# Kernel optimization log

Hardware: AMD Instinct MI355X
Metric: run time of the kernel (lower is better)

## Reference

```python
import jax, jax.numpy as jnp
import numpy as np

WINDOW = 16  # signature_window_size
D = 6        # input_path_dim


def _mlp(x, Ws, bs, final_act):
    for W, b in zip(Ws[:-1], bs[:-1]):
        x = jax.nn.softplus(W @ x + b)
    return final_act(Ws[-1] @ x + bs[-1])


def _windowed_logsig(xs):
    """Depth-2 log-signature of each window of the (piecewise-linear) path.
    Returns level-1 increments [n, D] and Levy areas [n, D, D] (antisymmetric)."""
    dx = xs[1:] - xs[:-1]                              # [T-1, D]
    n = dx.shape[0] // WINDOW
    dxw = dx[: n * WINDOW].reshape(n, WINDOW, D)
    lvl1 = dxw.sum(axis=1)                             # [n, D]
    cum = jnp.cumsum(dxw, axis=1) - dxw                # exclusive prefix sums
    cross = jnp.einsum('nwi,nwj->nij', cum, dxw)
    area = 0.5 * (cross - jnp.swapaxes(cross, 1, 2))   # [n, D, D]
    return lvl1, area


def setup_inputs() -> dict:
    key = jax.random.key(0)
    ks = jax.random.split(key, 9)
    S, H, OUT = 128, 128, 10
    B, T = 8, 513

    def lin(k, o, i):
        return jax.random.normal(k, (o, i), jnp.float32) / np.sqrt(i)

    return {
        'x': jax.random.normal(ks[0], (B, T, D), jnp.float32),
        'W_i0': lin(ks[1], H, D), 'b_i0': jnp.zeros((H,), jnp.float32),
        'W_i1': lin(ks[2], H, H), 'b_i1': jnp.zeros((H,), jnp.float32),
        'W_i2': lin(ks[3], S, H), 'b_i2': jnp.zeros((S,), jnp.float32),
        'W_v0': lin(ks[4], H, S), 'b_v0': jnp.zeros((H,), jnp.float32),
        'W_v1': lin(ks[5], H, H), 'b_v1': jnp.zeros((H,), jnp.float32),
        'W_v2': lin(ks[6], D * S, H), 'b_v2': jnp.zeros((D * S,), jnp.float32),
        'W_r': lin(ks[7], OUT, S), 'b_r': jnp.zeros((OUT,), jnp.float32),
    }


def reference(x, W_i0, b_i0, W_i1, b_i1, W_i2, b_i2,
              W_v0, b_v0, W_v1, b_v1, W_v2, b_v2, W_r, b_r):
    S = W_i2.shape[0]
    init_mlp = lambda z: _mlp(z, (W_i0, W_i1, W_i2), (b_i0, b_i1, b_i2), lambda u: u)
    # Vector fields V_i: R^S -> R^S, one per input channel (split_multi_vector_field)
    vf = lambda h: _mlp(h, (W_v0, W_v1, W_v2), (b_v0, b_v1, b_v2), jnp.tanh).reshape(D, S)
    mask = jnp.triu(jnp.ones((D, D), x.dtype), 1)  # Lyndon words i<j at depth 2

    def single(xs):  # xs: [T, D]
        lvl1, area = _windowed_logsig(xs)
        h0 = init_mlp(xs[0])

        def step(h, sig):
            l1, a = sig
            V = vf(h)                                  # [D, S]
            J = jax.jacfwd(vf)(h)                      # [D, S, S], J[j,b,a]=dV_j[b]/dh[a]
            M = jnp.einsum('jba,ia->ijb', J, V)        # (DV_j)(h) V_i(h)
            brack = M - jnp.swapaxes(M, 0, 1)          # Lie brackets [V_i, V_j](h)
            h_new = h + jnp.einsum('i,ib->b', l1, V) \
                      + jnp.einsum('ij,ijb->b', a * mask, brack)  # log-ODE step
            return h_new, h_new

        _, hist = jax.lax.scan(step, h0, (lvl1, area))
        hist = jnp.concatenate([h0[None], hist], axis=0)   # [n+1, S]
        return hist @ W_r.T + b_r                          # evolving readout

    return jax.vmap(single)(x)
```

## Files before the change

### kernel.cpp

```cpp
#include <hip/hip_runtime.h>
#include <math.h>

#define D    6
#define S    128
#define H    128
#define WIN  16
#define BB   8
#define TT   513
#define NW   32
#define OUTD 10

__device__ float g_lvl1[BB * NW * D];
__device__ float g_area[BB * NW * D * D];
__device__ float g_h0[BB * S];
__device__ float g_hist[BB * (NW + 1) * S];
__device__ float4 g_W2p[3 * 16 * 512];

__device__ __forceinline__ float sp(float x) {
    return (x > 20.f) ? x : log1pf(expf(x));
}
__device__ __forceinline__ float sigm(float x) {
    return 1.f / (1.f + expf(-x));
}
__device__ __forceinline__ float dot4(float4 a, float4 b, float acc) {
    return fmaf(a.x, b.x, fmaf(a.y, b.y, fmaf(a.z, b.z, fmaf(a.w, b.w, acc))));
}

#define O_W0   0
#define O_W1   16384
#define O_PS   32768
#define O_U    35840
#define O_T    36608
#define O_V    37376
#define O_H    38144
#define O_U1   38400
#define O_U2   38528
#define O_SG1  38656
#define O_SG2  38784
#define O_B0   38912
#define O_B1   39040
#define O_SIG  39168
#define O_B2   39256
#define SMTOT  40024

__global__ __launch_bounds__(512) void k_pack(const float* __restrict__ Wv2) {
    const float4* W24 = (const float4*)Wv2;
    int e = blockIdx.x * 512 + threadIdx.x;
    if (e < 3 * 16 * 512) {
        int ptr = e >> 13;
        int rem = e & 8191;
        int i   = rem >> 9;
        int tid = rem & 511;
        int r0 = tid >> 1, kh = tid & 1;
        int row = r0 + ptr * 256;
        g_W2p[e] = W24[row * 32 + kh * 16 + i];
    }
}

__global__ __launch_bounds__(256) void k_sig(
        const float* __restrict__ x,
        const float* __restrict__ Wi0, const float* __restrict__ bi0,
        const float* __restrict__ Wi1, const float* __restrict__ bi1,
        const float* __restrict__ Wi2, const float* __restrict__ bi2) {
    const int b = blockIdx.x;
    const int tid = threadIdx.x;
    __shared__ float dxs[NW][WIN][D];
    __shared__ float cums[NW][WIN][D];
    __shared__ float ua[H], ub[H];

    const float* xb = x + (size_t)b * TT * D;

    if (tid < NW * D) {
        int w = tid / D, i = tid % D;
        float run = 0.f;
        float prev = xb[(w * WIN) * D + i];
        for (int k = 0; k < WIN; ++k) {
            float cur = xb[(w * WIN + k + 1) * D + i];
            float d = cur - prev; prev = cur;
            dxs[w][k][i] = d;
            cums[w][k][i] = run;
            run += d;
        }
        g_lvl1[(b * NW + w) * D + i] = run;
    }
    __syncthreads();
    for (int e = tid; e < NW * D * D; e += blockDim.x) {
        int w = e / (D * D); int rem = e % (D * D);
        int i = rem / D, j = rem % D;
        float s = 0.f;
        for (int k = 0; k < WIN; ++k)
            s += cums[w][k][i] * dxs[w][k][j] - cums[w][k][j] * dxs[w][k][i];
        g_area[(b * NW + w) * (D * D) + rem] = 0.5f * s;
    }
    if (tid < H) {
        float z = bi0[tid];
        for (int k = 0; k < D; ++k) z += Wi0[tid * D + k] * xb[k];
        ua[tid] = sp(z);
    }
    __syncthreads();
    if (tid < H) {
        float z = bi1[tid];
        for (int k = 0; k < H; ++k) z += Wi1[tid * H + k] * ua[k];
        ub[tid] = sp(z);
    }
    __syncthreads();
    if (tid < H) {
        float z = bi2[tid];
        for (int k = 0; k < H; ++k) z += Wi2[tid * H + k] * ub[k];
        g_h0[b * S + tid] = z;
    }
}

__global__ __launch_bounds__(512, 2) void k_scan(
        const float* __restrict__ bv0, const float* __restrict__ bv1,
        const float* __restrict__ bv2,
        const float* __restrict__ Wv0, const float* __restrict__ Wv1) {
    __shared__ float sm[SMTOT];
    const int tid = threadIdx.x;
    const int b = blockIdx.x;
    const int r   = tid & 127;
    const int c4  = tid >> 7;
    const int key = r & 7;
    const int kh = tid & 1;
    const int r0 = tid >> 1, r1 = r0 + 256, r2 = r0 + 512;
    const int jA = tid >> 8, jB = 2 + jA, jC = 4 + jA;

    {
        float4* d = (float4*)(sm + O_W0);
        const float4* s0 = (const float4*)Wv0;
        const float4* s1 = (const float4*)Wv1;
        for (int i = tid; i < 4096; i += 512) { d[i] = s0[i]; d[4096 + i] = s1[i]; }
        sm[O_B2 + tid] = bv2[tid];
        if (tid < 256) sm[O_B2 + 512 + tid] = bv2[512 + tid];
        if (tid < 128) { sm[O_B0 + tid] = bv0[tid]; sm[O_B1 + tid] = bv1[tid]; }
    }
    const float4* WAp = g_W2p + tid;
    const float4* WBp = g_W2p + 8192 + tid;
    const float4* WCp = g_W2p + 16384 + tid;
    if (tid < 128) {
        float h0v = g_h0[b * 128 + tid];
        sm[O_H + tid] = h0v;
        g_hist[(b * (NW + 1)) * 128 + tid] = h0v;
    }
    if (tid >= 448) {
        int q = tid - 448;
        if (q < 42)
            sm[O_SIG + q] = (q < 6) ? g_lvl1[(b * NW) * 6 + q]
                                    : g_area[(b * NW) * 36 + q - 6];
    }
    __syncthreads();

    const float4* W04 = (const float4*)(sm + O_W0);
    const float4* W14 = (const float4*)(sm + O_W1);

    for (int t = 0; t < NW; ++t) {
        float rsig = 0.f;
        if (tid >= 448) {
            int q = tid - 448;
            if (q < 42 && t + 1 < NW)
                rsig = (q < 6) ? g_lvl1[(b * NW + t + 1) * 6 + q]
                               : g_area[(b * NW + t + 1) * 36 + q - 6];
        }
        const int sb = O_SIG + (t & 1) * 44;

        {
            float a = 0.f;
            const float4* H4 = (const float4*)(sm + O_H);
            #pragma unroll
            for (int q = 0; q < 8; ++q) {
                int qq = c4 * 8 + (q ^ key);
                a = dot4(W04[r * 32 + qq], H4[qq], a);
            }
            sm[O_PS + (c4 * 6) * 128 + r] = a;
        }
        __syncthreads();
        if (tid < 128) {
            float z = sm[O_B0 + tid];
            #pragma unroll
            for (int c = 0; c < 4; ++c) z += sm[O_PS + (c * 6) * 128 + tid];
            sm[O_U1 + tid] = sp(z); sm[O_SG1 + tid] = sigm(z);
        }
        __syncthreads();
        {
            float a = 0.f;
            const float4* U14 = (const float4*)(sm + O_U1);
            #pragma unroll
            for (int q = 0; q < 8; ++q) {
                int qq = c4 * 8 + (q ^ key);
                a = dot4(W14[r * 32 + qq], U14[qq], a);
            }
            sm[O_PS + (c4 * 6) * 128 + r] = a;
        }
        __syncthreads();
        if (tid < 128) {
            float z = sm[O_B1 + tid];
            #pragma unroll
            for (int c = 0; c < 4; ++c) z += sm[O_PS + (c * 6) * 128 + tid];
            sm[O_U2 + tid] = sp(z); sm[O_SG2 + tid] = sigm(z);
        }
        __syncthreads();
        {
            float acc0 = 0.f, acc1 = 0.f, acc2 = 0.f;
            const float4* U24 = (const float4*)(sm + O_U2) + kh * 16;
            #pragma unroll 4
            for (int i = 0; i < 16; ++i) {
                float4 u = U24[i];
                acc0 = dot4(WAp[i * 512], u, acc0);
                acc1 = dot4(WBp[i * 512], u, acc1);
                acc2 = dot4(WCp[i * 512], u, acc2);
            }
            sm[O_PS + kh * 768 + r0] = acc0;
            sm[O_PS + kh * 768 + r1] = acc1;
            sm[O_PS + kh * 768 + r2] = acc2;
        }
        __syncthreads();
        {
            sm[O_V + tid] = tanhf(sm[O_B2 + tid] + sm[O_PS + tid] + sm[O_PS + 768 + tid]);
            if (tid < 256) {
                int e = tid + 512;
                sm[O_V + e] = tanhf(sm[O_B2 + e] + sm[O_PS + e] + sm[O_PS + 768 + e]);
            }
        }
        __syncthreads();
        {
            float a0 = 0.f, a1 = 0.f, a2 = 0.f, a3 = 0.f, a4 = 0.f, a5 = 0.f;
            const float4* V4 = (const float4*)(sm + O_V);
            #pragma unroll
            for (int q = 0; q < 8; ++q) {
                int qq = c4 * 8 + (q ^ key);
                float4 w = W04[r * 32 + qq];
                a0 = dot4(w, V4[qq], a0);
                a1 = dot4(w, V4[32 + qq], a1);
                a2 = dot4(w, V4[64 + qq], a2);
                a3 = dot4(w, V4[96 + qq], a3);
                a4 = dot4(w, V4[128 + qq], a4);
                a5 = dot4(w, V4[160 + qq], a5);
            }
            sm[O_PS + (c4 * 6 + 0) * 128 + r] = a0;
            sm[O_PS + (c4 * 6 + 1) * 128 + r] = a1;
            sm[O_PS + (c4 * 6 + 2) * 128 + r] = a2;
            sm[O_PS + (c4 * 6 + 3) * 128 + r] = a3;
            sm[O_PS + (c4 * 6 + 4) * 128 + r] = a4;
            sm[O_PS + (c4 * 6 + 5) * 128 + r] = a5;
        }
        __syncthreads();
        {
            #pragma unroll
            for (int s = 0; s < 2; ++s) {
                int e = tid + s * 512;
                if (s == 0 || tid < 256) {
                    int jj = e >> 7, rr = e & 127;
                    float y0 = sm[O_PS + 0 * 128 + rr] + sm[O_PS + (6 + 0) * 128 + rr]
                             + sm[O_PS + (12 + 0) * 128 + rr] + sm[O_PS + (18 + 0) * 128 + rr];
                    float y1 = sm[O_PS + 1 * 128 + rr] + sm[O_PS + (6 + 1) * 128 + rr]
                             + sm[O_PS + (12 + 1) * 128 + rr] + sm[O_PS + (18 + 1) * 128 + rr];
                    float y2 = sm[O_PS + 2 * 128 + rr] + sm[O_PS + (6 + 2) * 128 + rr]
                             + sm[O_PS + (12 + 2) * 128 + rr] + sm[O_PS + (18 + 2) * 128 + rr];
                    float y3 = sm[O_PS + 3 * 128 + rr] + sm[O_PS + (6 + 3) * 128 + rr]
                             + sm[O_PS + (12 + 3) * 128 + rr] + sm[O_PS + (18 + 3) * 128 + rr];
                    float y4 = sm[O_PS + 4 * 128 + rr] + sm[O_PS + (6 + 4) * 128 + rr]
                             + sm[O_PS + (12 + 4) * 128 + rr] + sm[O_PS + (18 + 4) * 128 + rr];
                    float y5 = sm[O_PS + 5 * 128 + rr] + sm[O_PS + (6 + 5) * 128 + rr]
                             + sm[O_PS + (12 + 5) * 128 + rr] + sm[O_PS + (18 + 5) * 128 + rr];
                    const float* A0 = sm + sb + 6;
                    float sv = A0[0 * 6 + jj] * y0 + A0[1 * 6 + jj] * y1
                             + A0[2 * 6 + jj] * y2 + A0[3 * 6 + jj] * y3
                             + A0[4 * 6 + jj] * y4 + A0[5 * 6 + jj] * y5;
                    sm[O_T + jj * 128 + rr] = sm[O_SG1 + rr] * sv;
                }
            }
        }
        __syncthreads();
        {
            float a0 = 0.f, a1 = 0.f, a2 = 0.f, a3 = 0.f, a4 = 0.f, a5 = 0.f;
            const float4* T4 = (const float4*)(sm + O_T);
            #pragma unroll
            for (int q = 0; q < 8; ++q) {
                int qq = c4 * 8 + (q ^ key);
                float4 w = W14[r * 32 + qq];
                a0 = dot4(w, T4[qq], a0);
                a1 = dot4(w, T4[32 + qq], a1);
                a2 = dot4(w, T4[64 + qq], a2);
                a3 = dot4(w, T4[96 + qq], a3);
                a4 = dot4(w, T4[128 + qq], a4);
                a5 = dot4(w, T4[160 + qq], a5);
            }
            sm[O_PS + (c4 * 6 + 0) * 128 + r] = a0;
            sm[O_PS + (c4 * 6 + 1) * 128 + r] = a1;
            sm[O_PS + (c4 * 6 + 2) * 128 + r] = a2;
            sm[O_PS + (c4 * 6 + 3) * 128 + r] = a3;
            sm[O_PS + (c4 * 6 + 4) * 128 + r] = a4;
            sm[O_PS + (c4 * 6 + 5) * 128 + r] = a5;
        }
        __syncthreads();
        {
            #pragma unroll
            for (int s = 0; s < 2; ++s) {
                int e = tid + s * 512;
                if (s == 0 || tid < 256) {
                    int jj = e >> 7, rr = e & 127;
                    float sv = sm[O_PS + jj * 128 + rr] + sm[O_PS + (6 + jj) * 128 + rr]
                             + sm[O_PS + (12 + jj) * 128 + rr] + sm[O_PS + (18 + jj) * 128 + rr];
                    sm[O_U + jj * 128 + rr] = sm[O_SG2 + rr] * sv;
                }
            }
        }
        __syncthreads();
        {
            float acc0 = 0.f, acc1 = 0.f, acc2 = 0.f;
            const float4* TA = (const float4*)(sm + O_U) + jA * 32 + kh * 16;
            const float4* TB = (const float4*)(sm + O_U) + jB * 32 + kh * 16;
            const float4* TC = (const float4*)(sm + O_U) + jC * 32 + kh * 16;
            #pragma unroll 4
            for (int i = 0; i < 16; ++i) {
                acc0 = dot4(WAp[i * 512], TA[i], acc0);
                acc1 = dot4(WBp[i * 512], TB[i], acc1);
                acc2 = dot4(WCp[i * 512], TC[i], acc2);
            }
            sm[O_PS + kh * 768 + r0] = acc0;
            sm[O_PS + kh * 768 + r1] = acc1;
            sm[O_PS + kh * 768 + r2] = acc2;
        }
        __syncthreads();
        if (tid < 128) {
            float xh = sm[O_H + tid];
            #pragma unroll
            for (int i = 0; i < 6; ++i)
                xh = fmaf(sm[sb + i], sm[O_V + i * 128 + tid], xh);
            #pragma unroll
            for (int j = 0; j < 6; ++j) {
                float v = sm[O_V + j * 128 + tid];
                xh += (1.f - v * v) * (sm[O_PS + j * 128 + tid] + sm[O_PS + 768 + j * 128 + tid]);
            }
            sm[O_H + tid] = xh;
            g_hist[(b * (NW + 1) + t + 1) * 128 + tid] = xh;
        }
        if (tid >= 448) {
            int q = tid - 448;
            if (q < 42 && t + 1 < NW)
                sm[O_SIG + ((t + 1) & 1) * 44 + q] = rsig;
        }
        __syncthreads();
    }
}

__global__ __launch_bounds__(384) void k_read(const float* __restrict__ Wr,
                                              const float* __restrict__ br,
                                              float* __restrict__ out) {
    const int b = blockIdx.x, e = threadIdx.x;
    if (e < (NW + 1) * OUTD) {
        int t = e / OUTD, o = e % OUTD;
        float z = br[o];
        const float4* hrow = (const float4*)&g_hist[(b * (NW + 1) + t) * 128];
        const float4* wrow = (const float4*)&Wr[o * 128];
        float z0 = 0, z1 = 0, z2 = 0, z3 = 0;
        #pragma unroll 8
        for (int s4 = 0; s4 < 32; ++s4) {
            float4 hv = hrow[s4]; float4 wv = wrow[s4];
            z0 = fmaf(hv.x, wv.x, z0); z1 = fmaf(hv.y, wv.y, z1);
            z2 = fmaf(hv.z, wv.z, z2); z3 = fmaf(hv.w, wv.w, z3);
        }
        out[(b * (NW + 1) + t) * OUTD + o] = z + ((z0 + z1) + (z2 + z3));
    }
}

extern "C" void kernel_launch(void* const* d_in, const int* in_sizes, int n_in,
                              void* d_out, int out_size, void* d_ws, size_t ws_size,
                              hipStream_t stream) {
    const float* x   = (const float*)d_in[0];
    const float* Wi0 = (const float*)d_in[1];
    const float* bi0 = (const float*)d_in[2];
    const float* Wi1 = (const float*)d_in[3];
    const float* bi1 = (const float*)d_in[4];
    const float* Wi2 = (const float*)d_in[5];
    const float* bi2 = (const float*)d_in[6];
    const float* Wv0 = (const float*)d_in[7];
    const float* bv0 = (const float*)d_in[8];
    const float* Wv1 = (const float*)d_in[9];
    const float* bv1 = (const float*)d_in[10];
    const float* Wv2 = (const float*)d_in[11];
    const float* bv2 = (const float*)d_in[12];
    const float* Wr  = (const float*)d_in[13];
    const float* br  = (const float*)d_in[14];
    float* out = (float*)d_out;

    hipLaunchKernelGGL(k_pack, dim3(48), dim3(512), 0, stream, Wv2);
    hipLaunchKernelGGL(k_sig,  dim3(BB), dim3(256), 0, stream,
                       x, Wi0, bi0, Wi1, bi1, Wi2, bi2);
    hipLaunchKernelGGL(k_scan, dim3(BB), dim3(512), 0, stream,
                       bv0, bv1, bv2, Wv0, Wv1);
    hipLaunchKernelGGL(k_read, dim3(BB), dim3(384), 0, stream, Wr, br, out);
}
```

Baseline: 387.1 us.

## Remap tangent-propagation matvecs to two rows per thread and repack Wv2

Restructures the three per-step matvec stages of the Jacobian-vector propagation. The W0 and W1 matvecs now use 256 threads, each computing two output rows so each shared V/T load is reused twice. The final Wv2 stage uses 384 threads over a new full-K packed layout, which removes the split-K partial sum and one shared-memory add. It adds a second pack kernel and idles more threads per phase, trading parallelism for fewer shared loads and less reduction work on a latency-bound serial scan.

```diff
diff --git a/kernel.cpp b/kernel.cpp
--- a/kernel.cpp
+++ b/kernel.cpp
@@ -15,6 +15,7 @@
 __device__ float g_h0[BB * S];
 __device__ float g_hist[BB * (NW + 1) * S];
 __device__ float4 g_W2p[3 * 16 * 512];
+__device__ float4 g_W2p6[64 * 384];
 
 __device__ __forceinline__ float sp(float x) {
     return (x > 20.f) ? x : log1pf(expf(x));
@@ -57,6 +58,18 @@
     }
 }
 
+__global__ __launch_bounds__(512) void k_pack6(const float* __restrict__ Wv2) {
+    const float4* W24 = (const float4*)Wv2;
+    int e = blockIdx.x * 512 + threadIdx.x;
+    if (e < 64 * 384) {
+        int i = e / 384;
+        int t = e % 384;
+        int jb = t >> 6, pr = t & 63;
+        int row = jb * 128 + 2 * pr + (i >> 5);
+        g_W2p6[e] = W24[row * 32 + (i & 31)];
+    }
+}
+
 __global__ __launch_bounds__(256) void k_sig(
         const float* __restrict__ x,
         const float* __restrict__ Wi0, const float* __restrict__ bi0,
@@ -123,7 +136,11 @@
     const int key = r & 7;
     const int kh = tid & 1;
     const int r0 = tid >> 1, r1 = r0 + 256, r2 = r0 + 512;
-    const int jA = tid >> 8, jB = 2 + jA, jC = 4 + jA;
+    const int c4b = tid >> 6;
+    const int rp  = tid & 63;
+    const int keyb = rp & 7;
+    const int jb = tid >> 6;
+    const int pr = tid & 63;
 
     {
         float4* d = (float4*)(sm + O_W0);
@@ -222,104 +239,112 @@
             }
         }
         __syncthreads();
-        {
-            float a0 = 0.f, a1 = 0.f, a2 = 0.f, a3 = 0.f, a4 = 0.f, a5 = 0.f;
+        if (tid < 256) {
+            float aa0=0,aa1=0,aa2=0,aa3=0,aa4=0,aa5=0;
+            float bb0=0,bb1=0,bb2=0,bb3=0,bb4=0,bb5=0;
             const float4* V4 = (const float4*)(sm + O_V);
             #pragma unroll
             for (int q = 0; q < 8; ++q) {
-                int qq = c4 * 8 + (q ^ key);
-                float4 w = W04[r * 32 + qq];
-                a0 = dot4(w, V4[qq], a0);
-                a1 = dot4(w, V4[32 + qq], a1);
-                a2 = dot4(w, V4[64 + qq], a2);
-                a3 = dot4(w, V4[96 + qq], a3);
-                a4 = dot4(w, V4[128 + qq], a4);
-                a5 = dot4(w, V4[160 + qq], a5);
-            }
-            sm[O_PS + (c4 * 6 + 0) * 128 + r] = a0;
-            sm[O_PS + (c4 * 6 + 1) * 128 + r] = a1;
-            sm[O_PS + (c4 * 6 + 2) * 128 + r] = a2;
-            sm[O_PS + (c4 * 6 + 3) * 128 + r] = a3;
-            sm[O_PS + (c4 * 6 + 4) * 128 + r] = a4;
-            sm[O_PS + (c4 * 6 + 5) * 128 + r] = a5;
-        }
-        __syncthreads();
-        {
-            #pragma unroll
-            for (int s = 0; s < 2; ++s) {
-                int e = tid + s * 512;
-                if (s == 0 || tid < 256) {
-                    int jj = e >> 7, rr = e & 127;
-                    float y0 = sm[O_PS + 0 * 128 + rr] + sm[O_PS + (6 + 0) * 128 + rr]
-                             + sm[O_PS + (12 + 0) * 128 + rr] + sm[O_PS + (18 + 0) * 128 + rr];
-                    float y1 = sm[O_PS + 1 * 128 + rr] + sm[O_PS + (6 + 1) * 128 + rr]
-                             + sm[O_PS + (12 + 1) * 128 + rr] + sm[O_PS + (18 + 1) * 128 + rr];
-                    float y2 = sm[O_PS + 2 * 128 + rr] + sm[O_PS + (6 + 2) * 128 + rr]
-                             + sm[O_PS + (12 + 2) * 128 + rr] + sm[O_PS + (18 + 2) * 128 + rr];
-                    float y3 = sm[O_PS + 3 * 128 + rr] + sm[O_PS + (6 + 3) * 128 + rr]
-                             + sm[O_PS + (12 + 3) * 128 + rr] + sm[O_PS + (18 + 3) * 128 + rr];
-                    float y4 = sm[O_PS + 4 * 128 + rr] + sm[O_PS + (6 + 4) * 128 + rr]
-                             + sm[O_PS + (12 + 4) * 128 + rr] + sm[O_PS + (18 + 4) * 128 + rr];
-                    float y5 = sm[O_PS + 5 * 128 + rr] + sm[O_PS + (6 + 5) * 128 + rr]
-                             + sm[O_PS + (12 + 5) * 128 + rr] + sm[O_PS + (18 + 5) * 128 + rr];
-                    const float* A0 = sm + sb + 6;
-                    float sv = A0[0 * 6 + jj] * y0 + A0[1 * 6 + jj] * y1
-                             + A0[2 * 6 + jj] * y2 + A0[3 * 6 + jj] * y3
-                             + A0[4 * 6 + jj] * y4 + A0[5 * 6 + jj] * y5;
-                    sm[O_T + jj * 128 + rr] = sm[O_SG1 + rr] * sv;
-                }
-            }
-        }
-        __syncthreads();
-        {
-            float a0 = 0.f, a1 = 0.f, a2 = 0.f, a3 = 0.f, a4 = 0.f, a5 = 0.f;
+                int qq = c4b * 8 + (q ^ keyb);
+                float4 we = W04[(2 * rp) * 32 + qq];
+                float4 wo = W04[(2 * rp + 1) * 32 + qq];
+                float4 v0 = V4[qq];
+                float4 v1 = V4[32 + qq];
+                float4 v2 = V4[64 + qq];
+                float4 v3 = V4[96 + qq];
+                float4 v4 = V4[128 + qq];
+                float4 v5 = V4[160 + qq];
+                aa0 = dot4(we, v0, aa0); bb0 = dot4(wo, v0, bb0);
+                aa1 = dot4(we, v1, aa1); bb1 = dot4(wo, v1, bb1);
+                aa2 = dot4(we, v2, aa2); bb2 = dot4(wo, v2, bb2);
+                aa3 = dot4(we, v3, aa3); bb3 = dot4(wo, v3, bb3);
+                aa4 = dot4(we, v4, aa4); bb4 = dot4(wo, v4, bb4);
+                aa5 = dot4(we, v5, aa5); bb5 = dot4(wo, v5, bb5);
+            }
+            *(float2*)&sm[O_PS + (c4b * 6 + 0) * 128 + 2 * rp] = make_float2(aa0, bb0);
+            *(float2*)&sm[O_PS + (c4b * 6 + 1) * 128 + 2 * rp] = make_float2(aa1, bb1);
+            *(float2*)&sm[O_PS + (c4b * 6 + 2) * 128 + 2 * rp] = make_float2(aa2, bb2);
+            *(float2*)&sm[O_PS + (c4b * 6 + 3) * 128 + 2 * rp] = make_float2(aa3, bb3);
+            *(float2*)&sm[O_PS + (c4b * 6 + 4) * 128 + 2 * rp] = make_float2(aa4, bb4);
+            *(float2*)&sm[O_PS + (c4b * 6 + 5) * 128 + 2 * rp] = make_float2(aa5, bb5);
+        }
+        __syncthreads();
+        if (tid < 128) {
+            float y0 = sm[O_PS + 0 * 128 + tid] + sm[O_PS + 6 * 128 + tid]
+                     + sm[O_PS + 12 * 128 + tid] + sm[O_PS + 18 * 128 + tid];
+            float y1 = sm[O_PS + 1 * 128 + tid] + sm[O_PS + 7 * 128 + tid]
+                     + sm[O_PS + 13 * 128 + tid] + sm[O_PS + 19 * 128 + tid];
+            float y2 = sm[O_PS + 2 * 128 + tid] + sm[O_PS + 8 * 128 + tid]
+                     + sm[O_PS + 14 * 128 + tid] + sm[O_PS + 20 * 128 + tid];
+            float y3 = sm[O_PS + 3 * 128 + tid] + sm[O_PS + 9 * 128 + tid]
+                     + sm[O_PS + 15 * 128 + tid] + sm[O_PS + 21 * 128 + tid];
+            float y4 = sm[O_PS + 4 * 128 + tid] + sm[O_PS + 10 * 128 + tid]
+                     + sm[O_PS + 16 * 128 + tid] + sm[O_PS + 22 * 128 + tid];
+            float y5 = sm[O_PS + 5 * 128 + tid] + sm[O_PS + 11 * 128 + tid]
+                     + sm[O_PS + 17 * 128 + tid] + sm[O_PS + 23 * 128 + tid];
+            float sg = sm[O_SG1 + tid];
+            const float* A0 = sm + sb + 6;
+            #pragma unroll
+            for (int j = 0; j < 6; ++j) {
+                float sv = A0[0 * 6 + j] * y0 + A0[1 * 6 + j] * y1
+                         + A0[2 * 6 + j] * y2 + A0[3 * 6 + j] * y3
+                         + A0[4 * 6 + j] * y4 + A0[5 * 6 + j] * y5;
+                sm[O_T + j * 128 + tid] = sg * sv;
+            }
+        }
+        __syncthreads();
+        if (tid < 256) {
+            float aa0=0,aa1=0,aa2=0,aa3=0,aa4=0,aa5=0;
+            float bb0=0,bb1=0,bb2=0,bb3=0,bb4=0,bb5=0;
             const float4* T4 = (const float4*)(sm + O_T);
             #pragma unroll
             for (int q = 0; q < 8; ++q) {
-                int qq = c4 * 8 + (q ^ key);
-                float4 w = W14[r * 32 + qq];
-                a0 = dot4(w, T4[qq], a0);
-                a1 = dot4(w, T4[32 + qq], a1);
-                a2 = dot4(w, T4[64 + qq], a2);
-                a3 = dot4(w, T4[96 + qq], a3);
-                a4 = dot4(w, T4[128 + qq], a4);
-                a5 = dot4(w, T4[160 + qq], a5);
-            }
-            sm[O_PS + (c4 * 6 + 0) * 128 + r] = a0;
-            sm[O_PS + (c4 * 6 + 1) * 128 + r] = a1;
-            sm[O_PS + (c4 * 6 + 2) * 128 + r] = a2;
-            sm[O_PS + (c4 * 6 + 3) * 128 + r] = a3;
-            sm[O_PS + (c4 * 6 + 4) * 128 + r] = a4;
-            sm[O_PS + (c4 * 6 + 5) * 128 + r] = a5;
-        }
-        __syncthreads();
-        {
-            #pragma unroll
-            for (int s = 0; s < 2; ++s) {
-                int e = tid + s * 512;
-                if (s == 0 || tid < 256) {
-                    int jj = e >> 7, rr = e & 127;
-                    float sv = sm[O_PS + jj * 128 + rr] + sm[O_PS + (6 + jj) * 128 + rr]
-                             + sm[O_PS + (12 + jj) * 128 + rr] + sm[O_PS + (18 + jj) * 128 + rr];
-                    sm[O_U + jj * 128 + rr] = sm[O_SG2 + rr] * sv;
-                }
-            }
-        }
-        __syncthreads();
-        {
-            float acc0 = 0.f, acc1 = 0.f, acc2 = 0.f;
-            const float4* TA = (const float4*)(sm + O_U) + jA * 32 + kh * 16;
-            const float4* TB = (const float4*)(sm + O_U) + jB * 32 + kh * 16;
-            const float4* TC = (const float4*)(sm + O_U) + jC * 32 + kh * 16;
+                int qq = c4b * 8 + (q ^ keyb);
+                float4 we = W14[(2 * rp) * 32 + qq];
+                float4 wo = W14[(2 * rp + 1) * 32 + qq];
+                float4 v0 = T4[qq];
+                float4 v1 = T4[32 + qq];
+                float4 v2 = T4[64 + qq];
+                float4 v3 = T4[96 + qq];
+                float4 v4 = T4[128 + qq];
+                float4 v5 = T4[160 + qq];
+                aa0 = dot4(we, v0, aa0); bb0 = dot4(wo, v0, bb0);
+                aa1 = dot4(we, v1, aa1); bb1 = dot4(wo, v1, bb1);
+                aa2 = dot4(we, v2, aa2); bb2 = dot4(wo, v2, bb2);
+                aa3 = dot4(we, v3, aa3); bb3 = dot4(wo, v3, bb3);
+                aa4 = dot4(we, v4, aa4); bb4 = dot4(wo, v4, bb4);
+                aa5 = dot4(we, v5, aa5); bb5 = dot4(wo, v5, bb5);
+            }
+            *(float2*)&sm[O_PS + (c4b * 6 + 0) * 128 + 2 * rp] = make_float2(aa0, bb0);
+            *(float2*)&sm[O_PS + (c4b * 6 + 1) * 128 + 2 * rp] = make_float2(aa1, bb1);
+            *(float2*)&sm[O_PS + (c4b * 6 + 2) * 128 + 2 * rp] = make_float2(aa2, bb2);
+            *(float2*)&sm[O_PS + (c4b * 6 + 3) * 128 + 2 * rp] = make_float2(aa3, bb3);
+            *(float2*)&sm[O_PS + (c4b * 6 + 4) * 128 + 2 * rp] = make_float2(aa4, bb4);
+            *(float2*)&sm[O_PS + (c4b * 6 + 5) * 128 + 2 * rp] = make_float2(aa5, bb5);
+        }
+        __syncthreads();
+        if (tid < 128) {
+            float sg = sm[O_SG2 + tid];
+            #pragma unroll
+            for (int j = 0; j < 6; ++j) {
+                float sv = sm[O_PS + j * 128 + tid] + sm[O_PS + (6 + j) * 128 + tid]
+                         + sm[O_PS + (12 + j) * 128 + tid] + sm[O_PS + (18 + j) * 128 + tid];
+                sm[O_U + j * 128 + tid] = sg * sv;
+            }
+        }
+        __syncthreads();
+        if (tid < 384) {
+            float acc0 = 0.f, acc1 = 0.f;
+            const float4* T6 = (const float4*)(sm + O_U) + jb * 32;
+            const float4* W6a = g_W2p6 + tid;
+            const float4* W6b = g_W2p6 + 32 * 384 + tid;
             #pragma unroll 4
-            for (int i = 0; i < 16; ++i) {
-                acc0 = dot4(WAp[i * 512], TA[i], acc0);
-                acc1 = dot4(WBp[i * 512], TB[i], acc1);
-                acc2 = dot4(WCp[i * 512], TC[i], acc2);
-            }
-            sm[O_PS + kh * 768 + r0] = acc0;
-            sm[O_PS + kh * 768 + r1] = acc1;
-            sm[O_PS + kh * 768 + r2] = acc2;
+            for (int i = 0; i < 32; ++i) {
+                float4 tv = T6[i];
+                acc0 = dot4(W6a[i * 384], tv, acc0);
+                acc1 = dot4(W6b[i * 384], tv, acc1);
+            }
+            *(float2*)&sm[O_PS + jb * 128 + 2 * pr] = make_float2(acc0, acc1);
         }
         __syncthreads();
         if (tid < 128) {
@@ -330,7 +355,7 @@
             #pragma unroll
             for (int j = 0; j < 6; ++j) {
                 float v = sm[O_V + j * 128 + tid];
-                xh += (1.f - v * v) * (sm[O_PS + j * 128 + tid] + sm[O_PS + 768 + j * 128 + tid]);
+                xh += (1.f - v * v) * sm[O_PS + j * 128 + tid];
             }
             sm[O_H + tid] = xh;
             g_hist[(b * (NW + 1) + t + 1) * 128 + tid] = xh;
@@ -384,10 +409,11 @@
     const float* br  = (const float*)d_in[14];
     float* out = (float*)d_out;
 
-    hipLaunchKernelGGL(k_pack, dim3(48), dim3(512), 0, stream, Wv2);
-    hipLaunchKernelGGL(k_sig,  dim3(BB), dim3(256), 0, stream,
+    hipLaunchKernelGGL(k_pack,  dim3(48), dim3(512), 0, stream, Wv2);
+    hipLaunchKernelGGL(k_pack6, dim3(48), dim3(512), 0, stream, Wv2);
+    hipLaunchKernelGGL(k_sig,   dim3(BB), dim3(256), 0, stream,
                        x, Wi0, bi0, Wi1, bi1, Wi2, bi2);
-    hipLaunchKernelGGL(k_scan, dim3(BB), dim3(512), 0, stream,
+    hipLaunchKernelGGL(k_scan,  dim3(BB), dim3(512), 0, stream,
                        bv0, bv1, bv2, Wv0, Wv1);
-    hipLaunchKernelGGL(k_read, dim3(BB), dim3(384), 0, stream, Wr, br, out);
-}
+    hipLaunchKernelGGL(k_read,  dim3(BB), dim3(384), 0, stream, Wr, br, out);
+}
```

Result: slower. 419.6 us (+8.4%).
